# Optimization experiments

Hardware: AMD Instinct MI355X
Metric: run time of the kernel (lower is better)

Reference implementation:

```python
import jax, jax.numpy as jnp
import numpy as np

# dims: batch, q-heads, kv-heads, seq, head_dim, block size, window (kv blocks per q block)
B, H, KVH, S, D = 2, 16, 4, 4096, 64
BLK, W = 64, 8
G = H // KVH          # heads per group = 4
NQ = S // BLK         # 64 query blocks
L = W * BLK           # flattened kv window per q block = 512


def setup_inputs() -> dict:
    key = jax.random.key(0)
    k0, k1, k2, k3 = jax.random.split(key, 4)
    q = jax.random.normal(k0, (B, H, S, D), jnp.float32)
    k = jax.random.normal(k1, (B, KVH, S, D), jnp.float32)
    v = jax.random.normal(k2, (B, KVH, S, D), jnp.float32)
    # standard alibi slopes 2^(-8i/H)
    alibi_slopes = jnp.asarray(2.0 ** (-8.0 * np.arange(1, H + 1) / H), jnp.float32)
    # contiguous segments via sorted random ids
    segment_ids = jnp.sort(jax.random.randint(k3, (B, S), 0, 8, jnp.int32), axis=-1)
    # causal sliding window: q block qb attends to kv blocks [qb-W+1, qb]; -1 = invalid
    qb = np.arange(NQ)[:, None]
    bi = qb - (W - 1) + np.arange(W)[None, :]
    block_indices = jnp.asarray(np.where(bi < 0, -1, bi), jnp.int32)  # [NQ, W]
    return {"q": q, "k": k, "v": v, "alibi_slopes": alibi_slopes,
            "segment_ids": segment_ids, "block_indices": block_indices}


def reference(q, k, v, alibi_slopes, segment_ids, block_indices):
    scale = jnp.float32(1.0 / np.sqrt(D))
    NEG = jnp.float32(-1e30)

    qg = q.reshape(B, KVH, G, NQ, BLK, D)          # GQA grouping
    kb = k.reshape(B, KVH, NQ, BLK, D)
    vb = v.reshape(B, KVH, NQ, BLK, D)

    safe = jnp.clip(block_indices, 0)               # [NQ, W]
    kg = kb[:, :, safe]                             # [B,KVH,NQ,W,BLK,D] gathered kv blocks
    vg = vb[:, :, safe]

    pos_m = (jnp.arange(NQ) * BLK)[:, None] + jnp.arange(BLK)             # [NQ,BM]
    pos_n = safe[:, :, None] * BLK + jnp.arange(BLK)[None, None, :]       # [NQ,W,BN]

    valid = (block_indices >= 0)[:, None, :, None]                        # [NQ,1,W,1]
    causal = pos_m[:, :, None, None] >= pos_n[:, None, :, :]              # [NQ,BM,W,BN]
    seg_q = segment_ids.reshape(B, NQ, BLK)
    seg_k = jnp.take(segment_ids, pos_n.reshape(-1), axis=1).reshape(B, NQ, W, BLK)
    same_seg = (seg_q[:, :, :, None, None] == seg_k[:, :, None, :, :]) & (seg_q[:, :, :, None, None] >= 0)
    mask = ((valid & causal)[None] & same_seg)                            # [B,NQ,BM,W,BN]
    maskb = mask.reshape(B, 1, 1, NQ, BLK, L)                             # broadcast over KVH,G

    scores = jnp.einsum('bkgqmd,bkqwnd->bkgqmwn', qg, kg) * scale         # [B,KVH,G,NQ,BM,W,BN]
    pos_diff = jnp.abs(pos_m[:, :, None, None] - pos_n[:, None, :, :]).astype(jnp.float32)
    scores = scores - alibi_slopes.reshape(KVH, G)[None, :, :, None, None, None, None] * pos_diff
    scores = scores.reshape(B, KVH, G, NQ, BLK, L)
    scores = jnp.where(maskb, scores, NEG)

    row_max = jnp.max(scores, axis=-1, keepdims=True)
    p = jnp.where(maskb, jnp.exp(scores - row_max), 0.0)
    l = jnp.sum(p, axis=-1, keepdims=True)                                # [B,KVH,G,NQ,BM,1]
    vf = vg.reshape(B, KVH, NQ, L, D)
    acc = jnp.einsum('bkgqml,bkqld->bkgqmd', p, vf)
    out = jnp.where(l > 0, acc / jnp.where(l > 0, l, 1.0), 0.0)           # zero rows with no valid kv
    return out.reshape(B, H, S, D)
```

## Files before the change

kernel.cpp:

```cpp
#include <hip/hip_runtime.h>
#include <hip/hip_bf16.h>

#define NKVH 4
#define SEQ 4096
#define BLK 64
#define NW 8
#define NQB 64

typedef __attribute__((ext_vector_type(8))) short bf16x8;
typedef __attribute__((ext_vector_type(4))) float f32x4;

__device__ __forceinline__ unsigned pkbf(unsigned lo, unsigned hi) {
  return __builtin_amdgcn_perm(hi + 0x8000u, lo + 0x8000u, 0x07060302u);
}

__device__ __forceinline__ void gload16(const void* g, void* l) {
  __builtin_amdgcn_global_load_lds(
      (const __attribute__((address_space(1))) void*)g,
      (__attribute__((address_space(3))) void*)l, 16, 0, 0);
}

__global__ __launch_bounds__(256, 2)
void prep_kernel(const float* __restrict__ kp, const float* __restrict__ vp,
                 short* __restrict__ kw, short* __restrict__ vt)
{
  const int ki = blockIdx.x, kvh = blockIdx.y, b = blockIdx.z;
  const size_t base = (((size_t)(b*NKVH + kvh)*SEQ) + (size_t)ki*BLK)*64;
  __shared__ float sk[64][72];
  __shared__ float sv[64][72];
  const int t = threadIdx.x;
  #pragma unroll
  for (int it = 0; it < 4; ++it) {
    const int i = t + it*256;
    const int row = i >> 4, c4 = i & 15;
    float4 a = *(const float4*)(kp + base + row*64 + c4*4);
    *(float4*)&sk[row][c4*4] = a;
    float4 v = *(const float4*)(vp + base + row*64 + c4*4);
    *(float4*)&sv[row][c4*4] = v;
  }
  __syncthreads();
  #pragma unroll
  for (int it = 0; it < 2; ++it) {
    const int o = t + it*256;
    const int s = o >> 8, fd = (o >> 6) & 3, lg = (o >> 4) & 3, lr = o & 15;
    const int krow = 8*(lr >> 2) + (lr & 3) + 4*(fd & 1) + 32*(fd >> 1);
    const float* src = &sk[krow][s*32 + lg*8];
    uint4 w;
    w.x = pkbf(__float_as_uint(src[0]), __float_as_uint(src[1]));
    w.y = pkbf(__float_as_uint(src[2]), __float_as_uint(src[3]));
    w.z = pkbf(__float_as_uint(src[4]), __float_as_uint(src[5]));
    w.w = pkbf(__float_as_uint(src[6]), __float_as_uint(src[7]));
    *(uint4*)(kw + base + (size_t)o*8) = w;
    const int d = fd*16 + lr;
    const int n0 = s*32 + lg*8;
    uint4 u;
    u.x = pkbf(__float_as_uint(sv[n0+0][d]), __float_as_uint(sv[n0+1][d]));
    u.y = pkbf(__float_as_uint(sv[n0+2][d]), __float_as_uint(sv[n0+3][d]));
    u.z = pkbf(__float_as_uint(sv[n0+4][d]), __float_as_uint(sv[n0+5][d]));
    u.w = pkbf(__float_as_uint(sv[n0+6][d]), __float_as_uint(sv[n0+7][d]));
    *(uint4*)(vt + base + (size_t)o*8) = u;
  }
}

__global__ __launch_bounds__(512, 2)
void sattn_kernel(const float* __restrict__ qp, const short* __restrict__ kw,
                  const short* __restrict__ vt, const float* __restrict__ alibi,
                  const int* __restrict__ seg, const int* __restrict__ bidx,
                  float* __restrict__ outp)
{
  const int raw = blockIdx.x;
  const int xcd = raw & 7, li = raw >> 3;
  const int b = xcd >> 2, kvh = xcd & 3;
  const int qb = li & 63, hp = li >> 6;

  const int tid = threadIdx.x;
  const int wave = tid >> 6, lane = tid & 63;
  const int lr = lane & 15, lg = lane >> 4;
  const int wr = wave & 3, wh = wave >> 2;
  const int head = kvh*4 + hp*2 + wh;

  __shared__ short klds[2][4096];
  __shared__ short vlds[2][4096];

  int kis[NW];
  #pragma unroll
  for (int i = 0; i < NW; ++i) kis[i] = bidx[qb*NW + i];

  const int m_glob = qb*BLK + wr*16 + lr;
  const int mloc = wr*16 + lr;
  const int sq = seg[b*SEQ + m_glob];
  const float LOG2E = 1.4426950408889634f;
  const float nslope = -alibi[head] * LOG2E;

  const short* kbase = kw + ((size_t)(b*NKVH + kvh)*SEQ)*64;
  const short* vbase = vt + ((size_t)(b*NKVH + kvh)*SEQ)*64;

  auto STAGE = [&](int buf, int wi) {
    const int ki = kis[wi] < 0 ? 0 : kis[wi];
    gload16((const char*)(kbase + (size_t)ki*4096) + tid*16,
            (char*)&klds[buf][0] + wave*1024);
    gload16((const char*)(vbase + (size_t)ki*4096) + tid*16,
            (char*)&vlds[buf][0] + wave*1024);
  };

  STAGE(0, 0);

  bf16x8 qf[2];
  {
    const float qs = 0.125f * LOG2E;
    const float* qrow = qp + (((size_t)b*16 + head)*SEQ + m_glob)*64;
    #pragma unroll
    for (int s = 0; s < 2; ++s) {
      float4 a = *(const float4*)(qrow + s*32 + lg*8);
      float4 c = *(const float4*)(qrow + s*32 + lg*8 + 4);
      union { unsigned u[4]; bf16x8 v; } cv;
      cv.u[0] = pkbf(__float_as_uint(a.x*qs), __float_as_uint(a.y*qs));
      cv.u[1] = pkbf(__float_as_uint(a.z*qs), __float_as_uint(a.w*qs));
      cv.u[2] = pkbf(__float_as_uint(c.x*qs), __float_as_uint(c.y*qs));
      cv.u[3] = pkbf(__float_as_uint(c.z*qs), __float_as_uint(c.w*qs));
      qf[s] = cv.v;
    }
  }

  float lrun = 0.f;
  f32x4 oacc[4];
  #pragma unroll
  for (int dt = 0; dt < 4; ++dt) { f32x4 z = {0.f,0.f,0.f,0.f}; oacc[dt] = z; }

  __syncthreads();

  int cur = 0;
  #pragma unroll
  for (int wi = 0; wi < NW; ++wi) {
    if (wi + 1 < NW) STAGE(cur ^ 1, wi + 1);
    const int ki = kis[wi];
    if (ki >= 0) {
      f32x4 sacc[4];
      #pragma unroll
      for (int f = 0; f < 4; ++f) { f32x4 z = {0.f,0.f,0.f,0.f}; sacc[f] = z; }
      #pragma unroll
      for (int s = 0; s < 2; ++s) {
        bf16x8 kf[4];
        #pragma unroll
        for (int f = 0; f < 4; ++f)
          kf[f] = *(const bf16x8*)&klds[cur][(s*256 + f*64 + lane)*8];
        __builtin_amdgcn_s_setprio(1);
        #pragma unroll
        for (int f = 0; f < 4; ++f)
          sacc[f] = __builtin_amdgcn_mfma_f32_16x16x32_bf16(kf[f], qf[s], sacc[f], 0, 0, 0);
        __builtin_amdgcn_s_setprio(0);
      }

      unsigned pk[4][2];
      float psum = 0.f;
      #pragma unroll
      for (int f = 0; f < 4; ++f) {
        const int nb = lg*8 + 4*(f & 1) + 32*(f >> 1);
        const int4 s4 = *(const int4*)(seg + b*SEQ + ki*BLK + nb);
        const int skr[4] = {s4.x, s4.y, s4.z, s4.w};
        const float fbase = (float)(m_glob - ki*BLK - nb);
        float p[4];
        #pragma unroll
        for (int r = 0; r < 4; ++r) {
          bool dead = (skr[r] != sq);
          if (wi == NW-1) dead = dead || ((nb + r) > mloc);
          const float pd = dead ? 3.0e34f : (fbase - (float)r);
          p[r] = __builtin_amdgcn_exp2f(fmaf(nslope, pd, sacc[f][r]));
          psum += p[r];
        }
        pk[f][0] = pkbf(__float_as_uint(p[0]), __float_as_uint(p[1]));
        pk[f][1] = pkbf(__float_as_uint(p[2]), __float_as_uint(p[3]));
      }
      lrun += psum;

      #pragma unroll
      for (int s = 0; s < 2; ++s) {
        union { unsigned u[4]; bf16x8 v; } pf;
        pf.u[0] = pk[2*s][0]; pf.u[1] = pk[2*s][1];
        pf.u[2] = pk[2*s+1][0]; pf.u[3] = pk[2*s+1][1];
        bf16x8 vf[4];
        #pragma unroll
        for (int dt = 0; dt < 4; ++dt)
          vf[dt] = *(const bf16x8*)&vlds[cur][(s*256 + dt*64 + lane)*8];
        __builtin_amdgcn_s_setprio(1);
        #pragma unroll
        for (int dt = 0; dt < 4; ++dt)
          oacc[dt] = __builtin_amdgcn_mfma_f32_16x16x32_bf16(vf[dt], pf.v, oacc[dt], 0, 0, 0);
        __builtin_amdgcn_s_setprio(0);
      }
    }
    __syncthreads();
    cur ^= 1;
  }

  float lrow = lrun + __shfl_xor(lrun, 16);
  lrow += __shfl_xor(lrow, 32);
  const float inv = lrow > 0.f ? 1.f/lrow : 0.f;
  float* dst = outp + (((size_t)b*16 + head)*SEQ + m_glob)*64;
  #pragma unroll
  for (int dt = 0; dt < 4; ++dt) {
    float4 o;
    o.x = oacc[dt][0]*inv; o.y = oacc[dt][1]*inv;
    o.z = oacc[dt][2]*inv; o.w = oacc[dt][3]*inv;
    *(float4*)&dst[dt*16 + lg*4] = o;
  }
}

extern "C" void kernel_launch(void* const* d_in, const int* in_sizes, int n_in,
                              void* d_out, int out_size, void* d_ws, size_t ws_size,
                              hipStream_t stream) {
  const float* q    = (const float*)d_in[0];
  const float* k    = (const float*)d_in[1];
  const float* v    = (const float*)d_in[2];
  const float* al   = (const float*)d_in[3];
  const int*   sg   = (const int*)d_in[4];
  const int*   bi   = (const int*)d_in[5];
  short* kws  = (short*)d_ws;
  short* vtws = (short*)((char*)d_ws + (size_t)(1u<<22));
  dim3 pgrid(NQB, NKVH, 2);
  prep_kernel<<<pgrid, 256, 0, stream>>>(k, v, kws, vtws);
  sattn_kernel<<<dim3(1024), 512, 0, stream>>>(q, kws, vtws, al, sg, bi, (float*)d_out);
}
```

Baseline: 47.84 us.

## Halve block size so each wave handles two query row groups, compute row sums via MFMA

The attention kernel drops from 512 to 256 threads per block, and each wave now handles two 16-row query groups. K/V fragments loaded from LDS are reused across both groups, which halves LDS fragment traffic per MFMA. Segment ids are loaded once per kv block instead of once per group. The softmax row sum is now computed with an extra MFMA against a ones vector, replacing the scalar adds and cross-lane shuffles. In exchange there are fewer waves per block for latency hiding and higher register pressure from doubled accumulators.

```diff
diff --git a/kernel.cpp b/kernel.cpp
--- a/kernel.cpp
+++ b/kernel.cpp
@@ -62,7 +62,7 @@
   }
 }
 
-__global__ __launch_bounds__(512, 2)
+__global__ __launch_bounds__(256, 2)
 void sattn_kernel(const float* __restrict__ qp, const short* __restrict__ kw,
                   const short* __restrict__ vt, const float* __restrict__ alibi,
                   const int* __restrict__ seg, const int* __restrict__ bidx,
@@ -76,7 +76,7 @@
   const int tid = threadIdx.x;
   const int wave = tid >> 6, lane = tid & 63;
   const int lr = lane & 15, lg = lane >> 4;
-  const int wr = wave & 3, wh = wave >> 2;
+  const int wh = wave & 1, wq = wave >> 1;
   const int head = kvh*4 + hp*2 + wh;
 
   __shared__ short klds[2][4096];
@@ -86,9 +86,13 @@
   #pragma unroll
   for (int i = 0; i < NW; ++i) kis[i] = bidx[qb*NW + i];
 
-  const int m_glob = qb*BLK + wr*16 + lr;
-  const int mloc = wr*16 + lr;
-  const int sq = seg[b*SEQ + m_glob];
+  int m_glob[2], mloc[2], sq[2];
+  #pragma unroll
+  for (int g = 0; g < 2; ++g) {
+    mloc[g] = (wq*2 + g)*16 + lr;
+    m_glob[g] = qb*BLK + mloc[g];
+    sq[g] = seg[b*SEQ + m_glob[g]];
+  }
   const float LOG2E = 1.4426950408889634f;
   const float nslope = -alibi[head] * LOG2E;
 
@@ -97,35 +101,49 @@
 
   auto STAGE = [&](int buf, int wi) {
     const int ki = kis[wi] < 0 ? 0 : kis[wi];
-    gload16((const char*)(kbase + (size_t)ki*4096) + tid*16,
-            (char*)&klds[buf][0] + wave*1024);
-    gload16((const char*)(vbase + (size_t)ki*4096) + tid*16,
-            (char*)&vlds[buf][0] + wave*1024);
+    const char* ksrc = (const char*)(kbase + (size_t)ki*4096);
+    const char* vsrc = (const char*)(vbase + (size_t)ki*4096);
+    gload16(ksrc + tid*16,        (char*)&klds[buf][0] + wave*1024);
+    gload16(ksrc + 4096 + tid*16, (char*)&klds[buf][0] + 4096 + wave*1024);
+    gload16(vsrc + tid*16,        (char*)&vlds[buf][0] + wave*1024);
+    gload16(vsrc + 4096 + tid*16, (char*)&vlds[buf][0] + 4096 + wave*1024);
   };
 
   STAGE(0, 0);
 
-  bf16x8 qf[2];
+  bf16x8 qf[2][2];
   {
     const float qs = 0.125f * LOG2E;
-    const float* qrow = qp + (((size_t)b*16 + head)*SEQ + m_glob)*64;
     #pragma unroll
-    for (int s = 0; s < 2; ++s) {
-      float4 a = *(const float4*)(qrow + s*32 + lg*8);
-      float4 c = *(const float4*)(qrow + s*32 + lg*8 + 4);
-      union { unsigned u[4]; bf16x8 v; } cv;
-      cv.u[0] = pkbf(__float_as_uint(a.x*qs), __float_as_uint(a.y*qs));
-      cv.u[1] = pkbf(__float_as_uint(a.z*qs), __float_as_uint(a.w*qs));
-      cv.u[2] = pkbf(__float_as_uint(c.x*qs), __float_as_uint(c.y*qs));
-      cv.u[3] = pkbf(__float_as_uint(c.z*qs), __float_as_uint(c.w*qs));
-      qf[s] = cv.v;
+    for (int g = 0; g < 2; ++g) {
+      const float* qrow = qp + (((size_t)b*16 + head)*SEQ + m_glob[g])*64;
+      #pragma unroll
+      for (int s = 0; s < 2; ++s) {
+        float4 a = *(const float4*)(qrow + s*32 + lg*8);
+        float4 c = *(const float4*)(qrow + s*32 + lg*8 + 4);
+        union { unsigned u[4]; bf16x8 v; } cv;
+        cv.u[0] = pkbf(__float_as_uint(a.x*qs), __float_as_uint(a.y*qs));
+        cv.u[1] = pkbf(__float_as_uint(a.z*qs), __float_as_uint(a.w*qs));
+        cv.u[2] = pkbf(__float_as_uint(c.x*qs), __float_as_uint(c.y*qs));
+        cv.u[3] = pkbf(__float_as_uint(c.z*qs), __float_as_uint(c.w*qs));
+        qf[g][s] = cv.v;
+      }
     }
   }
 
-  float lrun = 0.f;
-  f32x4 oacc[4];
-  #pragma unroll
-  for (int dt = 0; dt < 4; ++dt) { f32x4 z = {0.f,0.f,0.f,0.f}; oacc[dt] = z; }
+  union { unsigned short us[8]; bf16x8 v; } one_u;
+  #pragma unroll
+  for (int i = 0; i < 8; ++i) one_u.us[i] = 0x3F80;
+  const bf16x8 onesf = one_u.v;
+
+  f32x4 oacc[2][4], osum[2];
+  #pragma unroll
+  for (int g = 0; g < 2; ++g) {
+    f32x4 z = {0.f,0.f,0.f,0.f};
+    osum[g] = z;
+    #pragma unroll
+    for (int dt = 0; dt < 4; ++dt) oacc[g][dt] = z;
+  }
 
   __syncthreads();
 
@@ -135,9 +153,19 @@
     if (wi + 1 < NW) STAGE(cur ^ 1, wi + 1);
     const int ki = kis[wi];
     if (ki >= 0) {
-      f32x4 sacc[4];
-      #pragma unroll
-      for (int f = 0; f < 4; ++f) { f32x4 z = {0.f,0.f,0.f,0.f}; sacc[f] = z; }
+      int skr[4][4];
+      #pragma unroll
+      for (int f = 0; f < 4; ++f) {
+        const int nb = lg*8 + 4*(f & 1) + 32*(f >> 1);
+        const int4 s4 = *(const int4*)(seg + b*SEQ + ki*BLK + nb);
+        skr[f][0] = s4.x; skr[f][1] = s4.y; skr[f][2] = s4.z; skr[f][3] = s4.w;
+      }
+
+      f32x4 sacc[2][4];
+      #pragma unroll
+      for (int g = 0; g < 2; ++g)
+        #pragma unroll
+        for (int f = 0; f < 4; ++f) { f32x4 z = {0.f,0.f,0.f,0.f}; sacc[g][f] = z; }
       #pragma unroll
       for (int s = 0; s < 2; ++s) {
         bf16x8 kf[4];
@@ -147,45 +175,54 @@
         __builtin_amdgcn_s_setprio(1);
         #pragma unroll
         for (int f = 0; f < 4; ++f)
-          sacc[f] = __builtin_amdgcn_mfma_f32_16x16x32_bf16(kf[f], qf[s], sacc[f], 0, 0, 0);
+          sacc[0][f] = __builtin_amdgcn_mfma_f32_16x16x32_bf16(kf[f], qf[0][s], sacc[0][f], 0, 0, 0);
+        #pragma unroll
+        for (int f = 0; f < 4; ++f)
+          sacc[1][f] = __builtin_amdgcn_mfma_f32_16x16x32_bf16(kf[f], qf[1][s], sacc[1][f], 0, 0, 0);
         __builtin_amdgcn_s_setprio(0);
       }
 
-      unsigned pk[4][2];
-      float psum = 0.f;
-      #pragma unroll
-      for (int f = 0; f < 4; ++f) {
-        const int nb = lg*8 + 4*(f & 1) + 32*(f >> 1);
-        const int4 s4 = *(const int4*)(seg + b*SEQ + ki*BLK + nb);
-        const int skr[4] = {s4.x, s4.y, s4.z, s4.w};
-        const float fbase = (float)(m_glob - ki*BLK - nb);
-        float p[4];
-        #pragma unroll
-        for (int r = 0; r < 4; ++r) {
-          bool dead = (skr[r] != sq);
-          if (wi == NW-1) dead = dead || ((nb + r) > mloc);
-          const float pd = dead ? 3.0e34f : (fbase - (float)r);
-          p[r] = __builtin_amdgcn_exp2f(fmaf(nslope, pd, sacc[f][r]));
-          psum += p[r];
+      unsigned pk[2][4][2];
+      #pragma unroll
+      for (int g = 0; g < 2; ++g) {
+        const float fdmb = (float)(m_glob[g] - ki*BLK);
+        #pragma unroll
+        for (int f = 0; f < 4; ++f) {
+          const int nb = lg*8 + 4*(f & 1) + 32*(f >> 1);
+          const float fbase = fdmb - (float)nb;
+          float p[4];
+          #pragma unroll
+          for (int r = 0; r < 4; ++r) {
+            bool dead = (skr[f][r] != sq[g]);
+            if (wi == NW-1) dead = dead || ((nb + r) > mloc[g]);
+            const float pd = dead ? 3.0e34f : (fbase - (float)r);
+            p[r] = __builtin_amdgcn_exp2f(fmaf(nslope, pd, sacc[g][f][r]));
+          }
+          pk[g][f][0] = pkbf(__float_as_uint(p[0]), __float_as_uint(p[1]));
+          pk[g][f][1] = pkbf(__float_as_uint(p[2]), __float_as_uint(p[3]));
         }
-        pk[f][0] = pkbf(__float_as_uint(p[0]), __float_as_uint(p[1]));
-        pk[f][1] = pkbf(__float_as_uint(p[2]), __float_as_uint(p[3]));
-      }
-      lrun += psum;
+      }
 
       #pragma unroll
       for (int s = 0; s < 2; ++s) {
-        union { unsigned u[4]; bf16x8 v; } pf;
-        pf.u[0] = pk[2*s][0]; pf.u[1] = pk[2*s][1];
-        pf.u[2] = pk[2*s+1][0]; pf.u[3] = pk[2*s+1][1];
         bf16x8 vf[4];
         #pragma unroll
         for (int dt = 0; dt < 4; ++dt)
           vf[dt] = *(const bf16x8*)&vlds[cur][(s*256 + dt*64 + lane)*8];
+        union { unsigned u[4]; bf16x8 v; } pf0, pf1;
+        pf0.u[0] = pk[0][2*s][0]; pf0.u[1] = pk[0][2*s][1];
+        pf0.u[2] = pk[0][2*s+1][0]; pf0.u[3] = pk[0][2*s+1][1];
+        pf1.u[0] = pk[1][2*s][0]; pf1.u[1] = pk[1][2*s][1];
+        pf1.u[2] = pk[1][2*s+1][0]; pf1.u[3] = pk[1][2*s+1][1];
         __builtin_amdgcn_s_setprio(1);
         #pragma unroll
         for (int dt = 0; dt < 4; ++dt)
-          oacc[dt] = __builtin_amdgcn_mfma_f32_16x16x32_bf16(vf[dt], pf.v, oacc[dt], 0, 0, 0);
+          oacc[0][dt] = __builtin_amdgcn_mfma_f32_16x16x32_bf16(vf[dt], pf0.v, oacc[0][dt], 0, 0, 0);
+        #pragma unroll
+        for (int dt = 0; dt < 4; ++dt)
+          oacc[1][dt] = __builtin_amdgcn_mfma_f32_16x16x32_bf16(vf[dt], pf1.v, oacc[1][dt], 0, 0, 0);
+        osum[0] = __builtin_amdgcn_mfma_f32_16x16x32_bf16(onesf, pf0.v, osum[0], 0, 0, 0);
+        osum[1] = __builtin_amdgcn_mfma_f32_16x16x32_bf16(onesf, pf1.v, osum[1], 0, 0, 0);
         __builtin_amdgcn_s_setprio(0);
       }
     }
@@ -193,16 +230,18 @@
     cur ^= 1;
   }
 
-  float lrow = lrun + __shfl_xor(lrun, 16);
-  lrow += __shfl_xor(lrow, 32);
-  const float inv = lrow > 0.f ? 1.f/lrow : 0.f;
-  float* dst = outp + (((size_t)b*16 + head)*SEQ + m_glob)*64;
-  #pragma unroll
-  for (int dt = 0; dt < 4; ++dt) {
-    float4 o;
-    o.x = oacc[dt][0]*inv; o.y = oacc[dt][1]*inv;
-    o.z = oacc[dt][2]*inv; o.w = oacc[dt][3]*inv;
-    *(float4*)&dst[dt*16 + lg*4] = o;
+  #pragma unroll
+  for (int g = 0; g < 2; ++g) {
+    const float lrow = osum[g][0];
+    const float inv = lrow > 0.f ? 1.f/lrow : 0.f;
+    float* dst = outp + (((size_t)b*16 + head)*SEQ + m_glob[g])*64;
+    #pragma unroll
+    for (int dt = 0; dt < 4; ++dt) {
+      float4 o;
+      o.x = oacc[g][dt][0]*inv; o.y = oacc[g][dt][1]*inv;
+      o.z = oacc[g][dt][2]*inv; o.w = oacc[g][dt][3]*inv;
+      *(float4*)&dst[dt*16 + lg*4] = o;
+    }
   }
 }
 
@@ -219,5 +258,5 @@
   short* vtws = (short*)((char*)d_ws + (size_t)(1u<<22));
   dim3 pgrid(NQB, NKVH, 2);
   prep_kernel<<<pgrid, 256, 0, stream>>>(k, v, kws, vtws);
-  sattn_kernel<<<dim3(1024), 512, 0, stream>>>(q, kws, vtws, al, sg, bi, (float*)d_out);
-}
+  sattn_kernel<<<dim3(1024), 256, 0, stream>>>(q, kws, vtws, al, sg, bi, (float*)d_out);
+}
```

Result: faster. 46.58 us (-2.6%).
